# Optimization experiments

Measured on AMD Instinct MI355X. Metric: run time of the kernel, lower is better.

## Reference

```python
import jax, jax.numpy as jnp
import numpy as np

LN_EPS = 1e-5

def _layer_norm(x, g, b):
    m = jnp.mean(x, axis=-1, keepdims=True)
    v = jnp.mean((x - m) ** 2, axis=-1, keepdims=True)
    return (x - m) / jnp.sqrt(v + LN_EPS) * g + b

def setup_inputs() -> dict:
    key = jax.random.key(0)
    ks = jax.random.split(key, 16)
    B, L, D = 4, 2048, 1024
    DF = 4 * D
    s_in = 1.0 / np.sqrt(D)
    s_ff = 1.0 / np.sqrt(DF)
    # torch init of phazor: exp(2j*pi*arange(D)/D) * |randn|
    ang = 2.0 * np.pi * jnp.arange(D, dtype=jnp.float32) / D
    mag = jnp.abs(jax.random.normal(ks[0], (D,), jnp.float32))
    return {
        "x": jax.random.normal(ks[1], (B, L, D), jnp.float32),
        "hidden_real": jax.random.normal(ks[2], (B, D), jnp.float32),
        "hidden_imag": jax.random.normal(ks[3], (B, D), jnp.float32),
        "phazor_real": mag * jnp.cos(ang),
        "phazor_imag": mag * jnp.sin(ang),
        "phazor_init_real": jax.random.normal(ks[4], (D,), jnp.float32),
        "phazor_init_imag": jax.random.normal(ks[5], (D,), jnp.float32),
        "ln_gamma": jnp.ones((D,), jnp.float32),
        "ln_beta": jnp.zeros((D,), jnp.float32),
        "fc_w": jax.random.uniform(ks[6], (D, D), jnp.float32, -s_in, s_in),
        "fc_b": jax.random.uniform(ks[7], (D,), jnp.float32, -s_in, s_in),
        "w1": jax.random.uniform(ks[8], (DF, D), jnp.float32, -s_in, s_in),
        "b1": jax.random.uniform(ks[9], (DF,), jnp.float32, -s_in, s_in),
        "w2": jax.random.uniform(ks[10], (D, DF), jnp.float32, -s_ff, s_ff),
        "b2": jax.random.uniform(ks[11], (D,), jnp.float32, -s_ff, s_ff),
    }

def _spiral_conv(x, hidden, phazor_p, phazor_init):
    # x: [B,L,D] real, hidden: [B,D] complex
    B, L, D = x.shape
    amag = jnp.abs(phazor_p)
    phazor = phazor_p / amag * jnp.exp(-amag)                      # [D]
    prog = jnp.power(phazor[None, :], jnp.arange(L)[:, None])      # [L,D]
    filt = prog * phazor_init[None, :]                             # [L,D]
    filt_fft = jnp.fft.fft(filt, n=2 * L, axis=0)                  # [2L,D]
    x_fft = jnp.fft.fft(x.astype(jnp.complex64), n=2 * L, axis=1)  # [B,2L,D]
    conv = jnp.fft.ifft(filt_fft[None] * x_fft, axis=1)[:, :L]     # [B,L,D]
    conv_with_past = conv + jax.lax.stop_gradient(hidden)[:, None, :] * prog[None] * phazor[None, None]
    return conv_with_past.real, conv_with_past

def reference(x, hidden_real, hidden_imag, phazor_real, phazor_imag,
              phazor_init_real, phazor_init_imag, ln_gamma, ln_beta,
              fc_w, fc_b, w1, b1, w2, b2):
    hidden = hidden_real + 1j * hidden_imag
    phazor_p = phazor_real + 1j * phazor_imag
    phazor_init = phazor_init_real + 1j * phazor_init_imag

    x_res = x
    xn = _layer_norm(x, ln_gamma, ln_beta)
    s, new_hidden = _spiral_conv(xn, hidden, phazor_p, phazor_init)
    y = jax.nn.silu(jnp.einsum('bld,ed->ble', x, fc_w) + fc_b)
    h = s * y + x_res                      # dropout is identity (p=0 / eval)
    hn = _layer_norm(h, ln_gamma, ln_beta) # same LayerNorm instance reused
    ffn = jnp.einsum('blf,df->bld', jax.nn.silu(jnp.einsum('bld,fd->blf', hn, w1) + b1), w2) + b2
    out = ffn + h
    return out, new_hidden
```

## Files before the change

kernel.cpp:

```cpp
#include <hip/hip_runtime.h>

typedef unsigned short u16;
typedef unsigned int u32;
typedef float f32x4 __attribute__((ext_vector_type(4)));
typedef __bf16 bf16x8 __attribute__((ext_vector_type(8)));

__device__ __forceinline__ float b2f(u16 u) {
    return __uint_as_float(((u32)u) << 16);
}
__device__ __forceinline__ u16 f2b(float f) {
    u32 u = __float_as_uint(f);
    return (u16)((u + 0x7FFFu + ((u >> 16) & 1u)) >> 16);
}
__device__ __forceinline__ bool is_f32(const u32* flag) {
    return flag[0] == 0x3F800000u;
}
__device__ __forceinline__ float lda(const void* p, size_t i, bool f) {
    return f ? ((const float*)p)[i] : b2f(((const u16*)p)[i]);
}
__device__ __forceinline__ void cmul(float& xr, float& xi, float yr, float yi) {
    float tr = xr * yr - xi * yi;
    xi = xr * yi + xi * yr;
    xr = tr;
}
__device__ __forceinline__ void gl2lds16(const void* g, void* l) {
    __builtin_amdgcn_global_load_lds(
        (const __attribute__((address_space(1))) void*)g,
        (__attribute__((address_space(3))) void*)l, 16, 0, 0);
}
__device__ __forceinline__ void wg_barrier() {
    asm volatile("" ::: "memory");
    __builtin_amdgcn_sched_barrier(0);
    __builtin_amdgcn_s_barrier();
    __builtin_amdgcn_sched_barrier(0);
    asm volatile("" ::: "memory");
}
#define VWAIT0 { asm volatile("s_waitcnt vmcnt(0)" ::: "memory"); __builtin_amdgcn_sched_barrier(0); }
#define VWAIT2 { asm volatile("s_waitcnt vmcnt(2)" ::: "memory"); __builtin_amdgcn_sched_barrier(0); }
#define VWAIT4 { asm volatile("s_waitcnt vmcnt(4)" ::: "memory"); __builtin_amdgcn_sched_barrier(0); }
#define VWAIT6 { asm volatile("s_waitcnt vmcnt(6)" ::: "memory"); __builtin_amdgcn_sched_barrier(0); }
#define LGKM0  { asm volatile("s_waitcnt lgkmcnt(0)" ::: "memory"); __builtin_amdgcn_sched_barrier(0); }

struct CvtArgs {
    const void* src[9];
    u16* dst[9];
    int n2[9];
    int tot;
};
__global__ __launch_bounds__(256) void cvtm_k(CvtArgs a, const u32* __restrict__ flag) {
    bool f = is_f32(flag);
    int i = blockIdx.x * 256 + threadIdx.x;
    if (i >= a.tot) return;
    int s = 0, base = 0;
    while (i - base >= a.n2[s]) { base += a.n2[s]; s++; }
    int k = i - base;
    if (f) {
        float2 v = ((const float2*)a.src[s])[k];
        ((u32*)a.dst[s])[k] = (u32)f2b(v.x) | ((u32)f2b(v.y) << 16);
    } else {
        ((u32*)a.dst[s])[k] = ((const u32*)a.src[s])[k];
    }
}

__global__ __launch_bounds__(256) void ln_k(const u16* __restrict__ x,
                                            const u16* __restrict__ g,
                                            const u16* __restrict__ be,
                                            u16* __restrict__ o, int D) {
    int row = blockIdx.x;
    const u16* xr = x + (size_t)row * D;
    int tid = threadIdx.x;
    float s = 0.f, s2 = 0.f;
    for (int i = tid; i < D; i += 256) {
        float v = b2f(xr[i]);
        s += v; s2 += v * v;
    }
    for (int off = 32; off > 0; off >>= 1) {
        s  += __shfl_down(s,  off, 64);
        s2 += __shfl_down(s2, off, 64);
    }
    __shared__ float red[8];
    int wave = tid >> 6;
    if ((tid & 63) == 0) { red[wave * 2] = s; red[wave * 2 + 1] = s2; }
    __syncthreads();
    if (tid == 0) {
        float ts = 0.f, ts2 = 0.f;
        for (int w = 0; w < 4; w++) { ts += red[w * 2]; ts2 += red[w * 2 + 1]; }
        float m = ts / D;
        float v = ts2 / D - m * m;
        red[0] = m;
        red[1] = rsqrtf(v + 1e-5f);
    }
    __syncthreads();
    float m = red[0], inv = red[1];
    u16* orow = o + (size_t)row * D;
    for (int i = tid; i < D; i += 256) {
        float v = (b2f(xr[i]) - m) * inv * b2f(g[i]) + b2f(be[i]);
        orow[i] = f2b(v);
    }
}

__global__ __launch_bounds__(256) void scan_partial_k(const u16* __restrict__ xn,
                                                      const void* __restrict__ phr_,
                                                      const void* __restrict__ phi_,
                                                      float2* __restrict__ T,
                                                      int L, int D, int C, int Kc,
                                                      const u32* __restrict__ flag) {
    bool f = is_f32(flag);
    int tid = blockIdx.x * 256 + threadIdx.x;
    int d = tid % D;
    int c = (tid / D) % C;
    int b = tid / (D * C);
    float pr = lda(phr_, d, f), pi = lda(phi_, d, f);
    float amag = fmaxf(sqrtf(pr * pr + pi * pi), 1e-12f);
    float sc = __expf(-amag) / amag;
    float phr = pr * sc, phi = pi * sc;
    float Tr = 0.f, Ti = 0.f;
    const u16* xp = xn + ((size_t)b * L + (size_t)c * Kc) * D + d;
    for (int t = 0; t < Kc; t++) {
        float x = b2f(xp[(size_t)t * D]);
        float nr = phr * Tr - phi * Ti + x;
        Ti = phr * Ti + phi * Tr;
        Tr = nr;
    }
    T[tid] = make_float2(Tr, Ti);
}

__global__ __launch_bounds__(256) void scan_prefix_k(const void* __restrict__ phr_,
                                                     const void* __restrict__ phi_,
                                                     const float2* __restrict__ T,
                                                     float2* __restrict__ E,
                                                     int D, int C,
                                                     const u32* __restrict__ flag) {
    bool f = is_f32(flag);
    int tid = blockIdx.x * 256 + threadIdx.x;
    int d = tid % D;
    int b = tid / D;
    float pr = lda(phr_, d, f), pi = lda(phi_, d, f);
    float amag = fmaxf(sqrtf(pr * pr + pi * pi), 1e-12f);
    float sc = __expf(-amag) / amag;
    float phr = pr * sc, phi = pi * sc;
    float kr = phr, ki = phi;
    for (int s = 0; s < 7; s++) cmul(kr, ki, kr, ki);
    float cr = 0.f, ci = 0.f;
    for (int c = 0; c < C; c++) {
        size_t i = ((size_t)b * C + c) * D + d;
        E[i] = make_float2(cr, ci);
        float2 t = T[i];
        cmul(cr, ci, kr, ki);
        cr += t.x; ci += t.y;
    }
}

__global__ __launch_bounds__(256) void scan_final_k(const u16* __restrict__ xn,
                                                    const void* __restrict__ phr_,
                                                    const void* __restrict__ phi_,
                                                    const void* __restrict__ pir_,
                                                    const void* __restrict__ pii_,
                                                    const void* __restrict__ hr_,
                                                    const void* __restrict__ hi_,
                                                    const float2* __restrict__ E,
                                                    u16* __restrict__ sws,
                                                    void* __restrict__ dout,
                                                    int MD, int out_elems,
                                                    int L, int D, int C, int Kc,
                                                    const u32* __restrict__ flag) {
    bool f = is_f32(flag);
    int tid = blockIdx.x * 256 + threadIdx.x;
    int d = tid % D;
    int c = (tid / D) % C;
    int b = tid / (D * C);
    float pr = lda(phr_, d, f), pi = lda(phi_, d, f);
    float amag = fmaxf(sqrtf(pr * pr + pi * pi), 1e-12f);
    float sc = __expf(-amag) / amag;
    float phr = pr * sc, phi = pi * sc;
    float kr = phr, ki = phi;
    for (int s = 0; s < 7; s++) cmul(kr, ki, kr, ki);
    float Pr = phr, Pi = phi;
    for (int j = 0; j < c; j++) cmul(Pr, Pi, kr, ki);
    float ir = lda(pir_, d, f), ii = lda(pii_, d, f);
    float hr = lda(hr_, (size_t)b * D + d, f), hi = lda(hi_, (size_t)b * D + d, f);
    float2 e = E[tid];
    float Sr = e.x, Si = e.y;
    const bool full = (out_elems >= 3 * MD);
    size_t mbase = (size_t)b * L + (size_t)c * Kc;
    for (int t = 0; t < Kc; t++) {
        size_t off = (mbase + t) * D + d;
        float x = b2f(xn[off]);
        float nr = phr * Sr - phi * Si + x;
        Si = phr * Si + phi * Sr;
        Sr = nr;
        float cr = ir * Sr - ii * Si + hr * Pr - hi * Pi;
        float ci = ir * Si + ii * Sr + hr * Pi + hi * Pr;
        sws[off] = f2b(cr);
        if (f) {
            float* fo = (float*)dout;
            if (full) {
                fo[(size_t)MD + 2 * off]     = cr;
                fo[(size_t)MD + 2 * off + 1] = ci;
            } else {
                fo[(size_t)MD + off] = cr;
            }
        } else {
            u16* uo = (u16*)dout;
            if (full) {
                uo[(size_t)MD + 2 * off]     = f2b(cr);
                uo[(size_t)MD + 2 * off + 1] = f2b(ci);
            } else {
                uo[(size_t)MD + off] = f2b(cr);
            }
        }
        cmul(Pr, Pi, phr, phi);
    }
}

template <int MODE, int BN>
__global__ __launch_bounds__(512) void gemm_nt(const u16* __restrict__ A,
                                               const u16* __restrict__ Bm,
                                               int M, int N, int K,
                                               const u16* __restrict__ bias,
                                               const u16* __restrict__ sbuf,
                                               const u16* __restrict__ xbuf,
                                               u16* __restrict__ out,
                                               void* __restrict__ outv,
                                               const u32* __restrict__ flag) {
    constexpr int NBUF = (BN == 256) ? 2 : 3;
    constexpr int MR   = (BN == 256) ? 8 : 4;
    __shared__ u16 As[NBUF][256 * 64];
    __shared__ u16 Bs[NBUF][BN * 64];
    const int tid = threadIdx.x;
    const int wave = tid >> 6, lane = tid & 63;
    const int quad = lane >> 4, l16 = lane & 15;

    const int NT = N / BN;
    const int j = blockIdx.x;
    const int gsize = 8 * NT;
    const int mg  = j / gsize;
    const int rem = j - mg * gsize;
    const int nt  = rem >> 3;
    const int mi  = rem & 7;
    const int bm = (mg * 8 + mi) * 256, bn = nt * BN;

    const int wrow = (BN == 256) ? (wave >> 2) * 128 : (wave >> 1) * 64;
    const int wcol = (BN == 256) ? (wave & 3) * 64   : (wave & 1) * 64;

    f32x4 acc[MR][4] = {};

    const int lr = lane >> 3;
    const int sl = (lane & 7) ^ lr;
    const size_t goff = (size_t)lr * K + sl * 8;
    const size_t K8 = (size_t)K * 8;
    const u16* aG = A  + (size_t)(bm + ((BN == 256) ? wave * 16 : wave * 32)) * K + goff;
    const u16* bG = Bm + (size_t)(bn + wave * 16) * K + goff;

#define STG_A(B_, t_, h_) { \
        const u16* ga = aG + (size_t)(t_) * 64 + (size_t)(h_) * 128 * K; \
        gl2lds16(ga,      &As[B_][((h_) * 128 + wave * 16) * 64]); \
        gl2lds16(ga + K8, &As[B_][((h_) * 128 + wave * 16 + 8) * 64]); }
#define STG_B(B_, t_, h_) { \
        const u16* gb = bG + (size_t)(t_) * 64 + (size_t)(h_) * 128 * K; \
        gl2lds16(gb,      &Bs[B_][((h_) * 128 + wave * 16) * 64]); \
        gl2lds16(gb + K8, &Bs[B_][((h_) * 128 + wave * 16 + 8) * 64]); }
#define STG_A128(B_, t_) { \
        const u16* ga = aG + (size_t)(t_) * 64; \
        gl2lds16(ga,          &As[B_][(wave * 32) * 64]); \
        gl2lds16(ga + K8,     &As[B_][(wave * 32 + 8) * 64]); \
        gl2lds16(ga + 2 * K8, &As[B_][(wave * 32 + 16) * 64]); \
        gl2lds16(ga + 3 * K8, &As[B_][(wave * 32 + 24) * 64]); }
#define STG_B128(B_, t_) { \
        const u16* gb = bG + (size_t)(t_) * 64; \
        gl2lds16(gb,      &Bs[B_][(wave * 16) * 64]); \
        gl2lds16(gb + K8, &Bs[B_][(wave * 16 + 8) * 64]); }

#define RDA(B_, m_, ks_) (*(const bf16x8*)&As[B_][(wrow + (m_) * 16 + l16) * 64 + \
        ((((ks_) * 4 + quad) ^ (l16 & 7)) << 3)])
#define RDB(B_, n_, ks_) (*(const bf16x8*)&Bs[B_][(wcol + (n_) * 16 + l16) * 64 + \
        ((((ks_) * 4 + quad) ^ (l16 & 7)) << 3)])

#define LDA4(RB, mh) { \
        av[0][0] = RDA(RB, (mh) * 4 + 0, 0); av[0][1] = RDA(RB, (mh) * 4 + 0, 1); \
        av[1][0] = RDA(RB, (mh) * 4 + 1, 0); av[1][1] = RDA(RB, (mh) * 4 + 1, 1); \
        av[2][0] = RDA(RB, (mh) * 4 + 2, 0); av[2][1] = RDA(RB, (mh) * 4 + 2, 1); \
        av[3][0] = RDA(RB, (mh) * 4 + 3, 0); av[3][1] = RDA(RB, (mh) * 4 + 3, 1); }
#define LDB2(RB, nh) { \
        bv[(nh) * 2 + 0][0] = RDB(RB, (nh) * 2 + 0, 0); \
        bv[(nh) * 2 + 0][1] = RDB(RB, (nh) * 2 + 0, 1); \
        bv[(nh) * 2 + 1][0] = RDB(RB, (nh) * 2 + 1, 0); \
        bv[(nh) * 2 + 1][1] = RDB(RB, (nh) * 2 + 1, 1); }

#define FM(mi_, ni_, ks_) acc[mi_][ni_] = __builtin_amdgcn_mfma_f32_16x16x32_bf16( \
        av[(mi_) & 3][ks_], bv[ni_][ks_], acc[mi_][ni_], 0, 0, 0)
#define MFMA16(mh, nh) { \
        __builtin_amdgcn_s_setprio(1); \
        FM((mh)*4+0, (nh)*2+0, 0); FM((mh)*4+0, (nh)*2+1, 0); \
        FM((mh)*4+1, (nh)*2+0, 0); FM((mh)*4+1, (nh)*2+1, 0); \
        FM((mh)*4+2, (nh)*2+0, 0); FM((mh)*4+2, (nh)*2+1, 0); \
        FM((mh)*4+3, (nh)*2+0, 0); FM((mh)*4+3, (nh)*2+1, 0); \
        FM((mh)*4+0, (nh)*2+0, 1); FM((mh)*4+0, (nh)*2+1, 1); \
        FM((mh)*4+1, (nh)*2+0, 1); FM((mh)*4+1, (nh)*2+1, 1); \
        FM((mh)*4+2, (nh)*2+0, 1); FM((mh)*4+2, (nh)*2+1, 1); \
        FM((mh)*4+3, (nh)*2+0, 1); FM((mh)*4+3, (nh)*2+1, 1); \
        __builtin_amdgcn_s_setprio(0); }
#define MFMA16K(ks_) { \
        __builtin_amdgcn_s_setprio(1); \
        FM(0, 0, ks_); FM(0, 1, ks_); FM(1, 0, ks_); FM(1, 1, ks_); \
        FM(0, 2, ks_); FM(0, 3, ks_); FM(1, 2, ks_); FM(1, 3, ks_); \
        FM(2, 0, ks_); FM(2, 1, ks_); FM(3, 0, ks_); FM(3, 1, ks_); \
        FM(2, 2, ks_); FM(2, 3, ks_); FM(3, 2, ks_); FM(3, 3, ks_); \
        __builtin_amdgcn_s_setprio(0); }

    bf16x8 av[4][2], bv[4][2];
    const int KT = K >> 6;

    if constexpr (BN == 256) {
        STG_A(0, 0, 0); STG_B(0, 0, 0); STG_B(0, 0, 1); STG_A(0, 0, 1);
        VWAIT4; wg_barrier();
#define TILE256(RB, SB, t_) { \
        const bool stg = (t_) + 1 < KT; \
         \
        LDA4(RB, 0); LDB2(RB, 0); \
        if (stg) STG_A(SB, (t_) + 1, 0);       \
        wg_barrier(); LGKM0; \
        MFMA16(0, 0); \
        if (stg) { VWAIT4 } else { VWAIT2 }    \
        wg_barrier(); \
         \
        LDB2(RB, 1); \
        if (stg) STG_B(SB, (t_) + 1, 0);       \
        wg_barrier(); LGKM0; \
        MFMA16(0, 1); \
        if (stg) { VWAIT4 } else { VWAIT0 }    \
        wg_barrier(); \
         \
        LDA4(RB, 1); \
        if (stg) STG_B(SB, (t_) + 1, 1);       \
        wg_barrier(); LGKM0; \
        MFMA16(1, 0); \
        wg_barrier(); \
         \
        if (stg) STG_A(SB, (t_) + 1, 1);       \
        wg_barrier(); LGKM0; \
        MFMA16(1, 1); \
        if (stg) { VWAIT4 }                    \
        wg_barrier(); }
        for (int t = 0; t < KT; t += 2) {
            TILE256(0, 1, t);
            TILE256(1, 0, t + 1);
        }
#undef TILE256
    } else {
        STG_A128(0, 0); STG_B128(0, 0);
        STG_A128(1, 1); STG_B128(1, 1);
        VWAIT6;
        wg_barrier();
#define TILE128(RB, SB, t_) { \
        const bool stg = (t_) + 2 < KT; \
         \
        av[0][0] = RDA(RB, 0, 0); av[1][0] = RDA(RB, 1, 0); \
        av[2][0] = RDA(RB, 2, 0); av[3][0] = RDA(RB, 3, 0); \
        bv[0][0] = RDB(RB, 0, 0); bv[1][0] = RDB(RB, 1, 0); \
        bv[2][0] = RDB(RB, 2, 0); bv[3][0] = RDB(RB, 3, 0); \
        if (stg) STG_A128(SB, (t_) + 2); \
        wg_barrier(); LGKM0; \
        MFMA16K(0); \
        wg_barrier(); \
         \
        av[0][1] = RDA(RB, 0, 1); av[1][1] = RDA(RB, 1, 1); \
        av[2][1] = RDA(RB, 2, 1); av[3][1] = RDA(RB, 3, 1); \
        bv[0][1] = RDB(RB, 0, 1); bv[1][1] = RDB(RB, 1, 1); \
        bv[2][1] = RDB(RB, 2, 1); bv[3][1] = RDB(RB, 3, 1); \
        if (stg) STG_B128(SB, (t_) + 2); \
        wg_barrier(); LGKM0; \
        MFMA16K(1); \
        if (stg) { VWAIT6 }                    \
        else if ((t_) + 1 < KT) { VWAIT0 }     \
        wg_barrier(); }
        for (int t = 0; t < KT; t += 3) {
            TILE128(0, 2, t);
            if (t + 1 < KT) TILE128(1, 0, t + 1);
            if (t + 2 < KT) TILE128(2, 1, t + 2);
        }
#undef TILE128
    }

    bool f = (MODE == 2) ? is_f32(flag) : false;
#pragma unroll
    for (int m = 0; m < MR; m++) {
#pragma unroll
        for (int n = 0; n < 4; n++) {
            int colg = bn + wcol + n * 16 + l16;
            float bsv = b2f(bias[colg]);
#pragma unroll
            for (int r = 0; r < 4; r++) {
                int rowg = bm + wrow + m * 16 + quad * 4 + r;
                size_t idx = (size_t)rowg * N + colg;
                float v = acc[m][n][r] + bsv;
                if (MODE == 0) {
                    float y = v / (1.f + __expf(-v));
                    float hv = b2f(sbuf[idx]) * y + b2f(xbuf[idx]);
                    out[idx] = f2b(hv);
                } else if (MODE == 1) {
                    float y = v / (1.f + __expf(-v));
                    out[idx] = f2b(y);
                } else {
                    float o = v + b2f(xbuf[idx]);
                    if (f) ((float*)outv)[idx] = o;
                    else   ((u16*)outv)[idx] = f2b(o);
                }
            }
        }
    }
#undef STG_A
#undef STG_B
#undef STG_A128
#undef STG_B128
#undef RDA
#undef RDB
#undef LDA4
#undef LDB2
#undef FM
#undef MFMA16
#undef MFMA16K
}

extern "C" void kernel_launch(void* const* d_in, const int* in_sizes, int n_in,
                              void* d_out, int out_size, void* d_ws, size_t ws_size,
                              hipStream_t stream) {
    const void* x   = d_in[0];
    const void* hr  = d_in[1];
    const void* hi  = d_in[2];
    const void* phr = d_in[3];
    const void* phi = d_in[4];
    const void* pir = d_in[5];
    const void* pii = d_in[6];
    const void* g   = d_in[7];
    const void* be  = d_in[8];
    const void* fcw = d_in[9];
    const void* fcb = d_in[10];
    const void* w1  = d_in[11];
    const void* b1  = d_in[12];
    const void* w2  = d_in[13];
    const void* b2  = d_in[14];
    const u32* flag = (const u32*)g;

    const int D  = in_sizes[3];
    const int Bb = in_sizes[1] / D;
    const int L  = in_sizes[0] / (Bb * D);
    const int DF = in_sizes[12];
    const int M  = Bb * L;
    const int Kc = 128, C = L / Kc;
    const int MD = M * D;

    char* ws = (char*)d_ws;
    size_t MD2 = (size_t)MD * 2;
    u16*    xb  = (u16*)(ws);
    u16*    xn  = (u16*)(ws + MD2);
    u16*    sws = (u16*)(ws + 2 * MD2);
    float2* T   = (float2*)(ws + 3 * MD2);
    float2* E   = (float2*)(ws + 3 * MD2 + (size_t)Bb * C * D * 8);
    u16*    a1  = (u16*)(ws);
    u16*    h   = (u16*)(ws + 4 * MD2);
    u16*    hn  = (u16*)(ws + 5 * MD2);
    char*   wp  = ws + 6 * MD2;
    u16* fcwb = (u16*)wp; wp += (size_t)D * D * 2;
    u16* w1b  = (u16*)wp; wp += (size_t)DF * D * 2;
    u16* w2b  = (u16*)wp; wp += (size_t)D * DF * 2;
    u16* fcbb = (u16*)wp; wp += (size_t)D * 2;
    u16* b1b  = (u16*)wp; wp += (size_t)DF * 2;
    u16* b2b  = (u16*)wp; wp += (size_t)D * 2;
    u16* gb   = (u16*)wp; wp += (size_t)D * 2;
    u16* bb   = (u16*)wp; wp += (size_t)D * 2;

    CvtArgs ca;
    const void* srcs[9] = { x, fcw, w1, w2, fcb, b1, b2, g, be };
    u16* dsts[9] = { xb, fcwb, w1b, w2b, fcbb, b1b, b2b, gb, bb };
    size_t ns[9] = { (size_t)MD, (size_t)D * D, (size_t)DF * D, (size_t)D * DF,
                     (size_t)D, (size_t)DF, (size_t)D, (size_t)D, (size_t)D };
    int tot = 0;
    for (int i = 0; i < 9; i++) {
        ca.src[i] = srcs[i];
        ca.dst[i] = dsts[i];
        ca.n2[i] = (int)(ns[i] / 2);
        tot += ca.n2[i];
    }
    ca.tot = tot;
    cvtm_k<<<(tot + 255) / 256, 256, 0, stream>>>(ca, flag);

    ln_k<<<M, 256, 0, stream>>>(xb, gb, bb, xn, D);
    scan_partial_k<<<(Bb * C * D) / 256, 256, 0, stream>>>(xn, phr, phi, T, L, D, C, Kc, flag);
    scan_prefix_k<<<(Bb * D) / 256, 256, 0, stream>>>(phr, phi, T, E, D, C, flag);
    scan_final_k<<<(Bb * C * D) / 256, 256, 0, stream>>>(xn, phr, phi, pir, pii, hr, hi,
                                                         E, sws, d_out, MD, out_size,
                                                         L, D, C, Kc, flag);
    gemm_nt<0, 128><<<(M / 256) * (D / 128), 512, 0, stream>>>(xb, fcwb, M, D, D, fcbb, sws, xb, h, nullptr, flag);
    ln_k<<<M, 256, 0, stream>>>(h, gb, bb, hn, D);
    gemm_nt<1, 256><<<(M / 256) * (DF / 256), 512, 0, stream>>>(hn, w1b, M, DF, D, b1b, nullptr, nullptr, a1, nullptr, flag);
    gemm_nt<2, 128><<<(M / 256) * (D / 128), 512, 0, stream>>>(a1, w2b, M, D, DF, b2b, nullptr, h, nullptr, d_out, flag);
}
```

Measured before the change: 462.8 us.

## Add 128x128-tile GEMM kernel for N=D GEMMs and vectorize LayerNorm loads

Adds a new 256-thread GEMM with 128x128 tiles and double-buffered LDS staging, and uses it for the fc and w2 GEMMs in place of the 256x128 tile path of gemm_nt. Those GEMMs now launch twice as many blocks, which should fill the CUs better at M=8192, N=1024. The price is more A/B reloads per output and a simpler single-barrier pipeline. LayerNorm also switches to 4-wide vector loads and stores, and the 128-wide branch is removed from gemm_nt.

```diff
diff --git a/kernel.cpp b/kernel.cpp
--- a/kernel.cpp
+++ b/kernel.cpp
@@ -4,6 +4,7 @@
 typedef unsigned int u32;
 typedef float f32x4 __attribute__((ext_vector_type(4)));
 typedef __bf16 bf16x8 __attribute__((ext_vector_type(8)));
+typedef unsigned short u16x4 __attribute__((ext_vector_type(4)));
 
 __device__ __forceinline__ float b2f(u16 u) {
     return __uint_as_float(((u32)u) << 16);
@@ -38,7 +39,6 @@
 #define VWAIT0 { asm volatile("s_waitcnt vmcnt(0)" ::: "memory"); __builtin_amdgcn_sched_barrier(0); }
 #define VWAIT2 { asm volatile("s_waitcnt vmcnt(2)" ::: "memory"); __builtin_amdgcn_sched_barrier(0); }
 #define VWAIT4 { asm volatile("s_waitcnt vmcnt(4)" ::: "memory"); __builtin_amdgcn_sched_barrier(0); }
-#define VWAIT6 { asm volatile("s_waitcnt vmcnt(6)" ::: "memory"); __builtin_amdgcn_sched_barrier(0); }
 #define LGKM0  { asm volatile("s_waitcnt lgkmcnt(0)" ::: "memory"); __builtin_amdgcn_sched_barrier(0); }
 
 struct CvtArgs {
@@ -70,9 +70,11 @@
     const u16* xr = x + (size_t)row * D;
     int tid = threadIdx.x;
     float s = 0.f, s2 = 0.f;
-    for (int i = tid; i < D; i += 256) {
-        float v = b2f(xr[i]);
-        s += v; s2 += v * v;
+    for (int i = tid * 4; i < D; i += 1024) {
+        u16x4 v = *(const u16x4*)&xr[i];
+        float a0 = b2f(v.x), a1 = b2f(v.y), a2 = b2f(v.z), a3 = b2f(v.w);
+        s  += (a0 + a1) + (a2 + a3);
+        s2 += (a0 * a0 + a1 * a1) + (a2 * a2 + a3 * a3);
     }
     for (int off = 32; off > 0; off >>= 1) {
         s  += __shfl_down(s,  off, 64);
@@ -93,9 +95,16 @@
     __syncthreads();
     float m = red[0], inv = red[1];
     u16* orow = o + (size_t)row * D;
-    for (int i = tid; i < D; i += 256) {
-        float v = (b2f(xr[i]) - m) * inv * b2f(g[i]) + b2f(be[i]);
-        orow[i] = f2b(v);
+    for (int i = tid * 4; i < D; i += 1024) {
+        u16x4 v = *(const u16x4*)&xr[i];
+        u16x4 gv = *(const u16x4*)&g[i];
+        u16x4 bv = *(const u16x4*)&be[i];
+        u16x4 r;
+        r.x = f2b((b2f(v.x) - m) * inv * b2f(gv.x) + b2f(bv.x));
+        r.y = f2b((b2f(v.y) - m) * inv * b2f(gv.y) + b2f(bv.y));
+        r.z = f2b((b2f(v.z) - m) * inv * b2f(gv.z) + b2f(bv.z));
+        r.w = f2b((b2f(v.w) - m) * inv * b2f(gv.w) + b2f(bv.w));
+        *(u16x4*)&orow[i] = r;
     }
 }
 
@@ -213,6 +222,129 @@
     }
 }
 
+template <int MODE>
+__global__ __launch_bounds__(256) void gemm128(const u16* __restrict__ A,
+                                               const u16* __restrict__ Bm,
+                                               int M, int N, int K,
+                                               const u16* __restrict__ bias,
+                                               const u16* __restrict__ sbuf,
+                                               const u16* __restrict__ xbuf,
+                                               u16* __restrict__ out,
+                                               void* __restrict__ outv,
+                                               const u32* __restrict__ flag) {
+    __shared__ u16 As[2][128 * 64];
+    __shared__ u16 Bs[2][128 * 64];
+    const int tid = threadIdx.x;
+    const int wave = tid >> 6, lane = tid & 63;
+    const int quad = lane >> 4, l16 = lane & 15;
+
+    const int NT = N >> 7;
+    const int j = blockIdx.x;
+    const int gsize = 8 * NT;
+    const int mg  = j / gsize;
+    const int rem = j - mg * gsize;
+    const int nt  = rem >> 3;
+    const int mi  = rem & 7;
+    const int bm = (mg * 8 + mi) * 128, bn = nt * 128;
+
+    const int wrow = (wave >> 1) * 64, wcol = (wave & 1) * 64;
+
+    f32x4 acc[4][4] = {};
+
+    const int lr = lane >> 3;
+    const int sl = (lane & 7) ^ lr;
+    const size_t goff = (size_t)lr * K + sl * 8;
+    const size_t K8 = (size_t)K * 8;
+    const u16* aG = A  + (size_t)(bm + wave * 32) * K + goff;
+    const u16* bG = Bm + (size_t)(bn + wave * 32) * K + goff;
+
+#define STG8(B_, t_) { \
+        const u16* ga = aG + (size_t)(t_) * 64; \
+        const u16* gb = bG + (size_t)(t_) * 64; \
+        gl2lds16(ga,          &As[B_][(wave * 32) * 64]); \
+        gl2lds16(ga + K8,     &As[B_][(wave * 32 + 8) * 64]); \
+        gl2lds16(ga + 2 * K8, &As[B_][(wave * 32 + 16) * 64]); \
+        gl2lds16(ga + 3 * K8, &As[B_][(wave * 32 + 24) * 64]); \
+        gl2lds16(gb,          &Bs[B_][(wave * 32) * 64]); \
+        gl2lds16(gb + K8,     &Bs[B_][(wave * 32 + 8) * 64]); \
+        gl2lds16(gb + 2 * K8, &Bs[B_][(wave * 32 + 16) * 64]); \
+        gl2lds16(gb + 3 * K8, &Bs[B_][(wave * 32 + 24) * 64]); }
+
+#define RD_A(B_, m_, ks_) (*(const bf16x8*)&As[B_][(wrow + (m_) * 16 + l16) * 64 + \
+        ((((ks_) * 4 + quad) ^ (l16 & 7)) << 3)])
+#define RD_B(B_, n_, ks_) (*(const bf16x8*)&Bs[B_][(wcol + (n_) * 16 + l16) * 64 + \
+        ((((ks_) * 4 + quad) ^ (l16 & 7)) << 3)])
+
+#define FMK(mm, nn, ks) acc[mm][nn] = __builtin_amdgcn_mfma_f32_16x16x32_bf16( \
+        av[mm][ks], bv[nn][ks], acc[mm][nn], 0, 0, 0)
+
+#define ITER128(CUR, t_) { \
+        const bool stg = (t_) + 1 < KT; \
+        if (stg) STG8(CUR ^ 1, (t_) + 1); \
+        av[0][0] = RD_A(CUR, 0, 0); av[1][0] = RD_A(CUR, 1, 0); \
+        av[2][0] = RD_A(CUR, 2, 0); av[3][0] = RD_A(CUR, 3, 0); \
+        bv[0][0] = RD_B(CUR, 0, 0); bv[1][0] = RD_B(CUR, 1, 0); \
+        bv[2][0] = RD_B(CUR, 2, 0); bv[3][0] = RD_B(CUR, 3, 0); \
+        av[0][1] = RD_A(CUR, 0, 1); av[1][1] = RD_A(CUR, 1, 1); \
+        av[2][1] = RD_A(CUR, 2, 1); av[3][1] = RD_A(CUR, 3, 1); \
+        bv[0][1] = RD_B(CUR, 0, 1); bv[1][1] = RD_B(CUR, 1, 1); \
+        bv[2][1] = RD_B(CUR, 2, 1); bv[3][1] = RD_B(CUR, 3, 1); \
+        FMK(0, 0, 0); FMK(0, 1, 0); FMK(1, 0, 0); FMK(1, 1, 0); \
+        FMK(0, 2, 0); FMK(0, 3, 0); FMK(1, 2, 0); FMK(1, 3, 0); \
+        FMK(2, 0, 0); FMK(2, 1, 0); FMK(3, 0, 0); FMK(3, 1, 0); \
+        FMK(2, 2, 0); FMK(2, 3, 0); FMK(3, 2, 0); FMK(3, 3, 0); \
+        FMK(0, 0, 1); FMK(0, 1, 1); FMK(1, 0, 1); FMK(1, 1, 1); \
+        FMK(0, 2, 1); FMK(0, 3, 1); FMK(1, 2, 1); FMK(1, 3, 1); \
+        FMK(2, 0, 1); FMK(2, 1, 1); FMK(3, 0, 1); FMK(3, 1, 1); \
+        FMK(2, 2, 1); FMK(2, 3, 1); FMK(3, 2, 1); FMK(3, 3, 1); \
+        if (stg) { VWAIT0 } \
+        wg_barrier(); }
+
+    bf16x8 av[4][2], bv[4][2];
+    const int KT = K >> 6;
+
+    STG8(0, 0);
+    VWAIT0; wg_barrier();
+
+    for (int t = 0; t < KT; t += 2) {
+        ITER128(0, t);
+        ITER128(1, t + 1);
+    }
+
+    bool f = (MODE == 2) ? is_f32(flag) : false;
+#pragma unroll
+    for (int m = 0; m < 4; m++) {
+#pragma unroll
+        for (int n = 0; n < 4; n++) {
+            int colg = bn + wcol + n * 16 + l16;
+            float bsv = b2f(bias[colg]);
+#pragma unroll
+            for (int r = 0; r < 4; r++) {
+                int rowg = bm + wrow + m * 16 + quad * 4 + r;
+                size_t idx = (size_t)rowg * N + colg;
+                float v = acc[m][n][r] + bsv;
+                if (MODE == 0) {
+                    float y = v / (1.f + __expf(-v));
+                    float hv = b2f(sbuf[idx]) * y + b2f(xbuf[idx]);
+                    out[idx] = f2b(hv);
+                } else if (MODE == 1) {
+                    float y = v / (1.f + __expf(-v));
+                    out[idx] = f2b(y);
+                } else {
+                    float o = v + b2f(xbuf[idx]);
+                    if (f) ((float*)outv)[idx] = o;
+                    else   ((u16*)outv)[idx] = f2b(o);
+                }
+            }
+        }
+    }
+#undef STG8
+#undef RD_A
+#undef RD_B
+#undef FMK
+#undef ITER128
+}
+
 template <int MODE, int BN>
 __global__ __launch_bounds__(512) void gemm_nt(const u16* __restrict__ A,
                                                const u16* __restrict__ Bm,
@@ -223,10 +355,8 @@
                                                u16* __restrict__ out,
                                                void* __restrict__ outv,
                                                const u32* __restrict__ flag) {
-    constexpr int NBUF = (BN == 256) ? 2 : 3;
-    constexpr int MR   = (BN == 256) ? 8 : 4;
-    __shared__ u16 As[NBUF][256 * 64];
-    __shared__ u16 Bs[NBUF][BN * 64];
+    __shared__ u16 As[2][256 * 64];
+    __shared__ u16 Bs[2][BN * 64];
     const int tid = threadIdx.x;
     const int wave = tid >> 6, lane = tid & 63;
     const int quad = lane >> 4, l16 = lane & 15;
@@ -240,16 +370,15 @@
     const int mi  = rem & 7;
     const int bm = (mg * 8 + mi) * 256, bn = nt * BN;
 
-    const int wrow = (BN == 256) ? (wave >> 2) * 128 : (wave >> 1) * 64;
-    const int wcol = (BN == 256) ? (wave & 3) * 64   : (wave & 1) * 64;
-
-    f32x4 acc[MR][4] = {};
+    const int wrow = (wave >> 2) * 128, wcol = (wave & 3) * 64;
+
+    f32x4 acc[8][4] = {};
 
     const int lr = lane >> 3;
     const int sl = (lane & 7) ^ lr;
     const size_t goff = (size_t)lr * K + sl * 8;
     const size_t K8 = (size_t)K * 8;
-    const u16* aG = A  + (size_t)(bm + ((BN == 256) ? wave * 16 : wave * 32)) * K + goff;
+    const u16* aG = A  + (size_t)(bm + wave * 16) * K + goff;
     const u16* bG = Bm + (size_t)(bn + wave * 16) * K + goff;
 
 #define STG_A(B_, t_, h_) { \
@@ -260,16 +389,6 @@
         const u16* gb = bG + (size_t)(t_) * 64 + (size_t)(h_) * 128 * K; \
         gl2lds16(gb,      &Bs[B_][((h_) * 128 + wave * 16) * 64]); \
         gl2lds16(gb + K8, &Bs[B_][((h_) * 128 + wave * 16 + 8) * 64]); }
-#define STG_A128(B_, t_) { \
-        const u16* ga = aG + (size_t)(t_) * 64; \
-        gl2lds16(ga,          &As[B_][(wave * 32) * 64]); \
-        gl2lds16(ga + K8,     &As[B_][(wave * 32 + 8) * 64]); \
-        gl2lds16(ga + 2 * K8, &As[B_][(wave * 32 + 16) * 64]); \
-        gl2lds16(ga + 3 * K8, &As[B_][(wave * 32 + 24) * 64]); }
-#define STG_B128(B_, t_) { \
-        const u16* gb = bG + (size_t)(t_) * 64; \
-        gl2lds16(gb,      &Bs[B_][(wave * 16) * 64]); \
-        gl2lds16(gb + K8, &Bs[B_][(wave * 16 + 8) * 64]); }
 
 #define RDA(B_, m_, ks_) (*(const bf16x8*)&As[B_][(wrow + (m_) * 16 + l16) * 64 + \
         ((((ks_) * 4 + quad) ^ (l16 & 7)) << 3)])
@@ -300,20 +419,12 @@
         FM((mh)*4+2, (nh)*2+0, 1); FM((mh)*4+2, (nh)*2+1, 1); \
         FM((mh)*4+3, (nh)*2+0, 1); FM((mh)*4+3, (nh)*2+1, 1); \
         __builtin_amdgcn_s_setprio(0); }
-#define MFMA16K(ks_) { \
-        __builtin_amdgcn_s_setprio(1); \
-        FM(0, 0, ks_); FM(0, 1, ks_); FM(1, 0, ks_); FM(1, 1, ks_); \
-        FM(0, 2, ks_); FM(0, 3, ks_); FM(1, 2, ks_); FM(1, 3, ks_); \
-        FM(2, 0, ks_); FM(2, 1, ks_); FM(3, 0, ks_); FM(3, 1, ks_); \
-        FM(2, 2, ks_); FM(2, 3, ks_); FM(3, 2, ks_); FM(3, 3, ks_); \
-        __builtin_amdgcn_s_setprio(0); }
 
     bf16x8 av[4][2], bv[4][2];
     const int KT = K >> 6;
 
-    if constexpr (BN == 256) {
-        STG_A(0, 0, 0); STG_B(0, 0, 0); STG_B(0, 0, 1); STG_A(0, 0, 1);
-        VWAIT4; wg_barrier();
+    STG_A(0, 0, 0); STG_B(0, 0, 0); STG_B(0, 0, 1); STG_A(0, 0, 1);
+    VWAIT4; wg_barrier();
 #define TILE256(RB, SB, t_) { \
         const bool stg = (t_) + 1 < KT; \
          \
@@ -342,49 +453,15 @@
         MFMA16(1, 1); \
         if (stg) { VWAIT4 }                    \
         wg_barrier(); }
-        for (int t = 0; t < KT; t += 2) {
-            TILE256(0, 1, t);
-            TILE256(1, 0, t + 1);
-        }
+    for (int t = 0; t < KT; t += 2) {
+        TILE256(0, 1, t);
+        TILE256(1, 0, t + 1);
+    }
 #undef TILE256
-    } else {
-        STG_A128(0, 0); STG_B128(0, 0);
-        STG_A128(1, 1); STG_B128(1, 1);
-        VWAIT6;
-        wg_barrier();
-#define TILE128(RB, SB, t_) { \
-        const bool stg = (t_) + 2 < KT; \
-         \
-        av[0][0] = RDA(RB, 0, 0); av[1][0] = RDA(RB, 1, 0); \
-        av[2][0] = RDA(RB, 2, 0); av[3][0] = RDA(RB, 3, 0); \
-        bv[0][0] = RDB(RB, 0, 0); bv[1][0] = RDB(RB, 1, 0); \
-        bv[2][0] = RDB(RB, 2, 0); bv[3][0] = RDB(RB, 3, 0); \
-        if (stg) STG_A128(SB, (t_) + 2); \
-        wg_barrier(); LGKM0; \
-        MFMA16K(0); \
-        wg_barrier(); \
-         \
-        av[0][1] = RDA(RB, 0, 1); av[1][1] = RDA(RB, 1, 1); \
-        av[2][1] = RDA(RB, 2, 1); av[3][1] = RDA(RB, 3, 1); \
-        bv[0][1] = RDB(RB, 0, 1); bv[1][1] = RDB(RB, 1, 1); \
-        bv[2][1] = RDB(RB, 2, 1); bv[3][1] = RDB(RB, 3, 1); \
-        if (stg) STG_B128(SB, (t_) + 2); \
-        wg_barrier(); LGKM0; \
-        MFMA16K(1); \
-        if (stg) { VWAIT6 }                    \
-        else if ((t_) + 1 < KT) { VWAIT0 }     \
-        wg_barrier(); }
-        for (int t = 0; t < KT; t += 3) {
-            TILE128(0, 2, t);
-            if (t + 1 < KT) TILE128(1, 0, t + 1);
-            if (t + 2 < KT) TILE128(2, 1, t + 2);
-        }
-#undef TILE128
-    }
 
     bool f = (MODE == 2) ? is_f32(flag) : false;
 #pragma unroll
-    for (int m = 0; m < MR; m++) {
+    for (int m = 0; m < 8; m++) {
 #pragma unroll
         for (int n = 0; n < 4; n++) {
             int colg = bn + wcol + n * 16 + l16;
@@ -411,15 +488,12 @@
     }
 #undef STG_A
 #undef STG_B
-#undef STG_A128
-#undef STG_B128
 #undef RDA
 #undef RDB
 #undef LDA4
 #undef LDB2
 #undef FM
 #undef MFMA16
-#undef MFMA16K
 }
 
 extern "C" void kernel_launch(void* const* d_in, const int* in_sizes, int n_in,
@@ -491,8 +565,8 @@
     scan_final_k<<<(Bb * C * D) / 256, 256, 0, stream>>>(xn, phr, phi, pir, pii, hr, hi,
                                                          E, sws, d_out, MD, out_size,
                                                          L, D, C, Kc, flag);
-    gemm_nt<0, 128><<<(M / 256) * (D / 128), 512, 0, stream>>>(xb, fcwb, M, D, D, fcbb, sws, xb, h, nullptr, flag);
+    gemm128<0><<<(M / 128) * (D / 128), 256, 0, stream>>>(xb, fcwb, M, D, D, fcbb, sws, xb, h, nullptr, flag);
     ln_k<<<M, 256, 0, stream>>>(h, gb, bb, hn, D);
     gemm_nt<1, 256><<<(M / 256) * (DF / 256), 512, 0, stream>>>(hn, w1b, M, DF, D, b1b, nullptr, nullptr, a1, nullptr, flag);
-    gemm_nt<2, 128><<<(M / 256) * (D / 128), 512, 0, stream>>>(a1, w2b, M, D, DF, b2b, nullptr, h, nullptr, d_out, flag);
-}
+    gemm128<2><<<(M / 128) * (D / 128), 256, 0, stream>>>(a1, w2b, M, D, DF, b2b, nullptr, h, nullptr, d_out, flag);
+}
```

Result: faster. 442.6 us (-4.4%).
